# Kernel tuning notes

Measured on AMD Instinct MI355X. Metric: run time of the kernel, lower is better.

## Reference

```python
import jax, jax.numpy as jnp
import numpy as np

B, N, K, NS = 2, 1024, 64, 32          # batch, points, keypoints (top-k), ball-query neighbors
RADIUS = 1.0                            # ball-query radius (sample_and_group)
R_VOX, S_VOX = 2.0, 0.4                 # voxelize search radius / step
NV = int(round(2 * R_VOX / S_VOX)) + 1  # 11 offsets per axis
C = NV ** 3                             # 1331 candidates per keypoint
F = 32                                  # deep feature channels (num_feat)


def _gather(data, idx):
    # data: (B, N, ...) ; idx: (B, ...) int -> (B, idx_shape..., ...)
    return jax.vmap(lambda d, i: d[i])(data, idx)


def setup_inputs() -> dict:
    key = jax.random.key(0)
    ks = jax.random.split(key, 16)
    f = lambda k, s: jax.random.normal(k, s, dtype=jnp.float32)
    return {
        "src_pts": f(ks[0], (B, 6, N)),
        "tgt_pts": f(ks[1], (B, 6, N)),
        "R_init": f(ks[2], (1, 3, 3)),
        "t_init": f(ks[3], (3, 1)),
        # feature-extraction shared MLP (6 -> 32 -> 32)
        "W1": f(ks[4], (6, F)) * 0.4, "b1": jnp.zeros((F,), jnp.float32),
        "W2": f(ks[5], (F, F)) * 0.2, "b2": jnp.zeros((F,), jnp.float32),
        # weighting (saliency) MLP (32 -> 16 -> 1)
        "Ww1": f(ks[6], (F, 16)) * 0.3, "bw1": jnp.zeros((16,), jnp.float32),
        "Ww2": f(ks[7], (16, 1)) * 0.3, "bw2": jnp.zeros((1,), jnp.float32),
        # deep-feature-embedding shared MLP (3+32 -> 32 -> 32)
        "Wd1": f(ks[8], (3 + F, F)) * 0.3, "bd1": jnp.zeros((F,), jnp.float32),
        "Wd2": f(ks[9], (F, F)) * 0.2, "bd2": jnp.zeros((F,), jnp.float32),
    }


def reference(src_pts, tgt_pts, R_init, t_init,
              W1, b1, W2, b2, Ww1, bw1, Ww2, bw2, Wd1, bd1, Wd2, bd2):
    def fe(pts):                                   # shared feature extraction (FE1)
        x = jnp.transpose(pts, (0, 2, 1))          # (B,N,6)
        h = jax.nn.relu(x @ W1 + b1)
        return x[..., :3], jax.nn.relu(h @ W2 + b2)  # xyz (B,N,3), feat (B,N,F)

    def dfe(x):                                    # shared DFE mini-PointNet MLP
        h = jax.nn.relu(x @ Wd1 + bd1)
        return jax.nn.relu(h @ Wd2 + bd2)

    src_xyz_all, src_feat = fe(src_pts)
    tgt_xyz_all, tgt_feat = fe(tgt_pts)

    # ---- weighting layer: per-point saliency, top-K keypoints ----
    score = (jax.nn.relu(src_feat @ Ww1 + bw1) @ Ww2 + bw2)[..., 0]  # (B,N)
    _, key_idx = jax.lax.top_k(score, K)                              # (B,K)

    src_pts_T = jnp.transpose(src_pts, (0, 2, 1))                     # (B,N,6)
    keypts = _gather(src_pts_T, key_idx)                              # (B,K,6)
    kxyz = keypts[..., :3]                                            # (B,K,3)

    # ---- sample_and_group: ball query among keypoints (npoint == K) ----
    sqd = jnp.sum((kxyz[:, :, None] - kxyz[:, None]) ** 2, -1)        # (B,K,K)
    gidx = jnp.broadcast_to(jnp.arange(K), (B, K, K))
    gidx = jnp.where(sqd > RADIUS ** 2, K, gidx)
    gidx = jnp.sort(gidx, -1)[:, :, :NS]
    gidx = jnp.where(gidx == K, gidx[:, :, :1], gidx)                 # (B,K,NS)

    grouped = _gather(kxyz, gidx)                                     # (B,K,NS,3)
    rel = grouped - kxyz[:, :, None]                                  # local coords
    orig_idx = _gather(key_idx, gidx)                                 # (B,K,NS) into N
    keyfeats = _gather(src_feat, orig_idx)                            # (B,K,NS,F)
    src_cat = jnp.concatenate([rel, keyfeats], -1)                    # (B,K,NS,3+F)

    # ---- voxelize: candidate grid around R_init-transformed keypoints ----
    Rm = jnp.broadcast_to(R_init, (B, 3, 3))
    kxyz_t = jnp.einsum('bij,bkj->bki', Rm, kxyz)                     # (B,K,3)
    off = jnp.linspace(-R_VOX, R_VOX, NV, dtype=jnp.float32)
    gx, gy, gz = jnp.meshgrid(off, off, off, indexing='ij')
    grid = jnp.stack([gx, gy, gz], -1).reshape(-1, 3)                 # (C,3)
    cand = kxyz_t[:, :, None, :] + grid                               # (B,K,C,3)

    # ---- 1-NN of each candidate in the target cloud (feature lookup) ----
    cn = jnp.sum(cand ** 2, -1)                                       # (B,K,C)
    tn = jnp.sum(tgt_xyz_all ** 2, -1)                                # (B,N)
    cross = jnp.einsum('bkcd,bnd->bkcn', cand, tgt_xyz_all)           # (B,K,C,N)
    d = cn[..., None] + tn[:, None, None, :] - 2.0 * cross
    nn = jnp.argmin(jax.lax.stop_gradient(d), -1)                     # (B,K,C)
    nn_xyz = _gather(tgt_xyz_all, nn)                                 # (B,K,C,3)
    nn_feat = _gather(tgt_feat, nn)                                   # (B,K,C,F)
    tgt_cat = jnp.concatenate([cand - nn_xyz, nn_feat], -1)           # (B,K,C,3+F)

    # ---- DFE embeddings + corresponding-point generation (CPG) ----
    src_emb = jnp.max(dfe(src_cat), axis=2)                           # (B,K,F)  max over neighbors
    tgt_emb = dfe(tgt_cat)                                            # (B,K,C,F)
    sim = jnp.einsum('bkd,bkcd->bkc', src_emb, tgt_emb)               # (B,K,C)
    w = jax.nn.softmax(sim, -1)
    tgt_vcp = jnp.einsum('bkc,bkcd->bkd', w, cand)                    # (B,K,3)

    return kxyz, tgt_vcp
```

## Files before the change

kernel.cpp:

```cpp
#include <hip/hip_runtime.h>
#include <math.h>

#define BB 2
#define NPTS 1024
#define KK 64
#define NSZ 32
#define CC 1331
#define FF 32
#define RAD2 1.0f
#define NCOL 121
#define NRNG 4

__global__ __launch_bounds__(64)
void k_features(const float* __restrict__ src_pts, const float* __restrict__ tgt_pts,
                const float* __restrict__ W1, const float* __restrict__ b1,
                const float* __restrict__ W2, const float* __restrict__ b2,
                const float* __restrict__ Ww1, const float* __restrict__ bw1,
                const float* __restrict__ Ww2, const float* __restrict__ bw2,
                const float* __restrict__ Wd1, const float* __restrict__ bd1,
                float* __restrict__ src_feat, float* __restrict__ tgt_A,
                float* __restrict__ tgt_m2, float* __restrict__ score)
{
    int gid = blockIdx.x * blockDim.x + threadIdx.x;
    int isTgt = gid >= BB * NPTS;
    int pn = gid & (BB * NPTS - 1);
    int b = pn >> 10, n = pn & 1023;
    const float* pts = isTgt ? tgt_pts : src_pts;
    float p[6];
#pragma unroll
    for (int i = 0; i < 6; i++) p[i] = pts[(b * 6 + i) * NPTS + n];
    float h[FF];
#pragma unroll
    for (int j = 0; j < FF; j++) {
        float a = b1[j];
#pragma unroll
        for (int i = 0; i < 6; i++) a = fmaf(p[i], W1[i * FF + j], a);
        h[j] = fmaxf(a, 0.0f);
    }
    float ft[FF];
#pragma unroll
    for (int j = 0; j < FF; j++) {
        float a = b2[j];
#pragma unroll
        for (int i = 0; i < FF; i++) a = fmaf(h[i], W2[i * FF + j], a);
        ft[j] = fmaxf(a, 0.0f);
    }
    if (isTgt) {
        float x = p[0], y = p[1], z = p[2];
        float4 v; v.x = x; v.y = y; v.z = z; v.w = x * x + y * y + z * z;
        ((float4*)tgt_m2)[b * NPTS + n] = v;
        float av[FF];
#pragma unroll
        for (int j = 0; j < FF; j++) av[j] = bd1[j];
#pragma unroll
        for (int i = 0; i < FF; i++) {
            float fi = ft[i];
#pragma unroll
            for (int j = 0; j < FF; j++)
                av[j] = fmaf(fi, Wd1[(3 + i) * FF + j], av[j]);
        }
#pragma unroll
        for (int j = 0; j < FF; j++) tgt_A[(b * NPTS + n) * FF + j] = av[j];
    } else {
#pragma unroll
        for (int j = 0; j < FF; j++) src_feat[(b * NPTS + n) * FF + j] = ft[j];
        float acc = bw2[0];
#pragma unroll
        for (int j = 0; j < 16; j++) {
            float a = bw1[j];
#pragma unroll
            for (int i = 0; i < FF; i++) a = fmaf(ft[i], Ww1[i * 16 + j], a);
            acc = fmaf(fmaxf(a, 0.0f), Ww2[j], acc);
        }
        score[b * NPTS + n] = acc;
    }
}

__global__ __launch_bounds__(256)
void k_rank(const float* __restrict__ score, const float* __restrict__ src_pts,
            const float* __restrict__ R,
            int* __restrict__ key_idx, float* __restrict__ kxyz,
            float* __restrict__ kxyz_t, float* __restrict__ out_kxyz)
{
    int blk = blockIdx.x;
    int b = blk >> 4;
    int pbase = (blk & 15) << 6;
    int t = threadIdx.x;
    int sub = t & 3;
    int lp = t >> 2;
    int n = pbase + lp;
    __shared__ float sc[NPTS];
    for (int i = t; i < NPTS; i += 256) sc[i] = score[b * NPTS + i];
    __syncthreads();
    float s = sc[n];
    int rank = 0;
#pragma unroll 8
    for (int jj = 0; jj < 256; jj++) {
        int j = (jj << 2) | sub;
        float sj = sc[j];
        bool before = (sj > s) || (sj == s && j < n);
        rank += before ? 1 : 0;
    }
    rank += __shfl_xor(rank, 1, 64);
    rank += __shfl_xor(rank, 2, 64);
    if (sub == 0 && rank < KK) {
        key_idx[b * KK + rank] = n;
        float x = src_pts[(b * 6 + 0) * NPTS + n];
        float y = src_pts[(b * 6 + 1) * NPTS + n];
        float z = src_pts[(b * 6 + 2) * NPTS + n];
        int o = (b * KK + rank) * 3;
        kxyz[o] = x; kxyz[o + 1] = y; kxyz[o + 2] = z;
        out_kxyz[o] = x; out_kxyz[o + 1] = y; out_kxyz[o + 2] = z;
#pragma unroll
        for (int i = 0; i < 3; i++)
            kxyz_t[o + i] = R[i * 3 + 0] * x + R[i * 3 + 1] * y + R[i * 3 + 2] * z;
    }
}

__global__ __launch_bounds__(256)
void k_scan(const float* __restrict__ kxyz_t, const float* __restrict__ tgt_m2,
            const float* __restrict__ kxyz, const int* __restrict__ key_idx,
            const float* __restrict__ src_feat,
            const float* __restrict__ Wd1, const float* __restrict__ bd1,
            const float* __restrict__ Wd2, const float* __restrict__ bd2,
            float2* __restrict__ part, float* __restrict__ src_emb)
{
    int bid = blockIdx.x;
    int bk = bid >> 2, r = bid & 3;
    int b = bk >> 6, kk = bk & 63;
    int t = threadIdx.x;
    int u = t >> 7, lt = t & 127;
    __shared__ float4 P[256];
    __shared__ float2 pbuf[2][NCOL][11];
    __shared__ float kxs[KK][3];
    __shared__ int gidx[NSZ];
    __shared__ float hb[NSZ][FF + 1];
    __shared__ float eb[NSZ][FF + 1];
    P[t] = ((const float4*)tgt_m2)[(b << 10) + (r << 8) + t];
    float kx = kxyz_t[bk * 3 + 0], ky = kxyz_t[bk * 3 + 1], kz = kxyz_t[bk * 3 + 2];
    float kx2 = -2.0f * kx, ky2 = -2.0f * ky, kz2 = -2.0f * kz;
    bool active = lt < NCOL;
    int pc = active ? lt : 0;
    int ixv = pc / 11, iyv = pc - ixv * 11;
    float gx2 = -2.0f * (-2.0f + ixv * 0.4f);
    float gy2 = -2.0f * (-2.0f + iyv * 0.4f);
    float gz2[11];
#pragma unroll
    for (int iz = 0; iz < 11; iz++) gz2[iz] = -2.0f * (-2.0f + iz * 0.4f);
    float best[11]; int bn[11];
#pragma unroll
    for (int iz = 0; iz < 11; iz++) { best[iz] = 3.0e38f; bn[iz] = 0; }
    __syncthreads();
    if (active) {
        const int pb = u << 7;
#pragma unroll 8
        for (int i = 0; i < 128; i++) {
            float4 v = P[pb + i];
            float a = fmaf(kx2, v.x, fmaf(ky2, v.y, fmaf(kz2, v.z, v.w)));
            float e = fmaf(gx2, v.x, fmaf(gy2, v.y, a));
#pragma unroll
            for (int iz = 0; iz < 11; iz++) {
                float d = fmaf(gz2[iz], v.z, e);
                bool l = d < best[iz];
                best[iz] = l ? d : best[iz];
                bn[iz] = l ? i : bn[iz];
            }
        }
#pragma unroll
        for (int iz = 0; iz < 11; iz++)
            pbuf[u][lt][iz] = make_float2(best[iz], __int_as_float(bn[iz] + (u << 7)));
    }
    __syncthreads();
    if (u == 0 && active) {
        int cbase = ((bk << 2) + r) * CC + lt * 11;
#pragma unroll
        for (int iz = 0; iz < 11; iz++) {
            float2 r0 = pbuf[0][lt][iz], r1 = pbuf[1][lt][iz];
            float2 m = (r1.x < r0.x) ? r1 : r0;
            part[cbase + iz] = make_float2(m.x,
                __int_as_float(__float_as_int(m.y) + (r << 8)));
        }
    }
    if (r != 0) return;
    if (t < KK) {
        kxs[t][0] = kxyz[(b * KK + t) * 3 + 0];
        kxs[t][1] = kxyz[(b * KK + t) * 3 + 1];
        kxs[t][2] = kxyz[(b * KK + t) * 3 + 2];
    }
    __syncthreads();
    if (t < KK) {
        float cx = kxs[kk][0], cy = kxs[kk][1], cz = kxs[kk][2];
        float dx = kxs[t][0] - cx, dy = kxs[t][1] - cy, dz = kxs[t][2] - cz;
        float sq = dx * dx + dy * dy + dz * dz;
        unsigned long long mask = __ballot(sq <= RAD2);
        if (t < NSZ) {
            int cnt = __popcll(mask);
            int want = (t < cnt) ? t : 0;
            unsigned long long mm = mask;
            for (int q = 0; q < want; q++) mm &= (mm - 1);
            gidx[t] = __ffsll(mm) - 1;
        }
    }
    __syncthreads();
    {
        int s = t >> 3, jb = (t & 7) << 2;
        int g = gidx[s];
        float cx = kxs[kk][0], cy = kxs[kk][1], cz = kxs[kk][2];
        float xr = kxs[g][0] - cx, yr = kxs[g][1] - cy, zr = kxs[g][2] - cz;
        int orig = key_idx[b * KK + g];
        const float* fz = &src_feat[(b * NPTS + orig) * FF];
        float fr[FF];
#pragma unroll
        for (int i = 0; i < FF; i++) fr[i] = fz[i];
#pragma unroll
        for (int jj = 0; jj < 4; jj++) {
            int j = jb + jj;
            float a = bd1[j];
            a = fmaf(xr, Wd1[0 * FF + j], a);
            a = fmaf(yr, Wd1[1 * FF + j], a);
            a = fmaf(zr, Wd1[2 * FF + j], a);
#pragma unroll
            for (int i = 0; i < FF; i++) a = fmaf(fr[i], Wd1[(3 + i) * FF + j], a);
            hb[s][j] = fmaxf(a, 0.0f);
        }
    }
    __syncthreads();
    {
        int s = t >> 3, jb = (t & 7) << 2;
#pragma unroll
        for (int jj = 0; jj < 4; jj++) {
            int j = jb + jj;
            float a = bd2[j];
#pragma unroll
            for (int i = 0; i < FF; i++) a = fmaf(hb[s][i], Wd2[i * FF + j], a);
            eb[s][j] = fmaxf(a, 0.0f);
        }
    }
    __syncthreads();
    if (t < FF) {
        float m = eb[0][t];
#pragma unroll
        for (int s2 = 1; s2 < NSZ; s2++) m = fmaxf(m, eb[s2][t]);
        src_emb[bk * FF + t] = m;
    }
}

__global__ __launch_bounds__(256)
void k_mlp(const float2* __restrict__ part, const float* __restrict__ kxyz_t,
           const float* __restrict__ tgt_m2, const float* __restrict__ tgt_A,
           const float* __restrict__ src_emb,
           const float* __restrict__ Wd1,
           const float* __restrict__ Wd2, const float* __restrict__ bd2,
           float* __restrict__ sim)
{
    const int NCH = 6;
    int bid = blockIdx.x;
    int chunk = bid % NCH;
    int bk = bid / NCH;
    int b = bk >> 6;
    int t = threadIdx.x;
    int c = chunk * 256 + t;
    int cc = min(c, CC - 1);
    float2 rb = part[(bk << 2) * CC + cc];
#pragma unroll
    for (int r = 1; r < NRNG; r++) {
        float2 o = part[((bk << 2) + r) * CC + cc];
        if (o.x < rb.x) rb = o;
    }
    int nb = __float_as_int(rb.y);
    float4 nv = ((const float4*)tgt_m2)[(b << 10) + nb];
    const float4* az = (const float4*)&tgt_A[((b << 10) + nb) * FF];
    float h[FF];
#pragma unroll
    for (int i = 0; i < FF / 4; i++) {
        float4 v = az[i];
        h[i * 4 + 0] = v.x; h[i * 4 + 1] = v.y; h[i * 4 + 2] = v.z; h[i * 4 + 3] = v.w;
    }
    int ixv = cc / 121, rem = cc - ixv * 121, iyv = rem / 11, izv = rem - iyv * 11;
    float cx = kxyz_t[bk * 3 + 0] + (-2.0f + ixv * 0.4f);
    float cy = kxyz_t[bk * 3 + 1] + (-2.0f + iyv * 0.4f);
    float cz = kxyz_t[bk * 3 + 2] + (-2.0f + izv * 0.4f);
    float x0 = cx - nv.x, x1 = cy - nv.y, x2 = cz - nv.z;
#pragma unroll
    for (int j = 0; j < FF; j++) {
        float a = h[j];
        a = fmaf(x0, Wd1[0 * FF + j], a);
        a = fmaf(x1, Wd1[1 * FF + j], a);
        a = fmaf(x2, Wd1[2 * FF + j], a);
        h[j] = fmaxf(a, 0.0f);
    }
    float sv = 0.0f;
#pragma unroll
    for (int j = 0; j < FF; j++) {
        float a = bd2[j];
#pragma unroll
        for (int i = 0; i < FF; i++) a = fmaf(h[i], Wd2[i * FF + j], a);
        sv = fmaf(fmaxf(a, 0.0f), src_emb[bk * FF + j], sv);
    }
    if (c < CC) sim[bk * CC + c] = sv;
}

__global__ __launch_bounds__(256)
void k_softmax(const float* __restrict__ sim, const float* __restrict__ kxyz_t,
               float* __restrict__ out_vcp)
{
    int bk = blockIdx.x;
    int t = threadIdx.x;
    __shared__ float red[256];
    __shared__ float4 red4[256];
    float kx = kxyz_t[bk * 3 + 0], ky = kxyz_t[bk * 3 + 1], kz = kxyz_t[bk * 3 + 2];
    float lm = -3.0e38f;
    for (int c = t; c < CC; c += 256) lm = fmaxf(lm, sim[bk * CC + c]);
    red[t] = lm;
    __syncthreads();
    for (int s2 = 128; s2 > 0; s2 >>= 1) {
        if (t < s2) red[t] = fmaxf(red[t], red[t + s2]);
        __syncthreads();
    }
    float m = red[0];
    float se = 0.f, sx = 0.f, sy = 0.f, sz = 0.f;
    for (int c = t; c < CC; c += 256) {
        float e = expf(sim[bk * CC + c] - m);
        int ix = c / 121, rem = c - ix * 121, iy = rem / 11, iz = rem - iy * 11;
        float cxx = kx + (-2.0f + ix * 0.4f);
        float cyy = ky + (-2.0f + iy * 0.4f);
        float czz = kz + (-2.0f + iz * 0.4f);
        se += e;
        sx = fmaf(e, cxx, sx);
        sy = fmaf(e, cyy, sy);
        sz = fmaf(e, czz, sz);
    }
    red4[t] = make_float4(se, sx, sy, sz);
    __syncthreads();
    for (int s2 = 128; s2 > 0; s2 >>= 1) {
        if (t < s2) {
            float4 a = red4[t], bq = red4[t + s2];
            red4[t] = make_float4(a.x + bq.x, a.y + bq.y, a.z + bq.z, a.w + bq.w);
        }
        __syncthreads();
    }
    if (t == 0) {
        float4 r = red4[0];
        out_vcp[bk * 3 + 0] = r.y / r.x;
        out_vcp[bk * 3 + 1] = r.z / r.x;
        out_vcp[bk * 3 + 2] = r.w / r.x;
    }
}

extern "C" void kernel_launch(void* const* d_in, const int* in_sizes, int n_in,
                              void* d_out, int out_size, void* d_ws, size_t ws_size,
                              hipStream_t stream)
{
    (void)in_sizes; (void)n_in; (void)out_size; (void)ws_size;
    const float* src_pts = (const float*)d_in[0];
    const float* tgt_pts = (const float*)d_in[1];
    const float* R_init  = (const float*)d_in[2];
    const float* W1  = (const float*)d_in[4];
    const float* b1  = (const float*)d_in[5];
    const float* W2  = (const float*)d_in[6];
    const float* b2  = (const float*)d_in[7];
    const float* Ww1 = (const float*)d_in[8];
    const float* bw1 = (const float*)d_in[9];
    const float* Ww2 = (const float*)d_in[10];
    const float* bw2 = (const float*)d_in[11];
    const float* Wd1 = (const float*)d_in[12];
    const float* bd1 = (const float*)d_in[13];
    const float* Wd2 = (const float*)d_in[14];
    const float* bd2 = (const float*)d_in[15];

    float* ws = (float*)d_ws;
    float* src_feat = ws;
    float* tgt_A    = src_feat + BB * NPTS * FF;
    float* tgt_m2   = tgt_A + BB * NPTS * FF;
    float* score    = tgt_m2 + BB * NPTS * 4;
    int*   key_idx  = (int*)(score + BB * NPTS);
    float* kxyz     = (float*)(key_idx + BB * KK);
    float* kxyz_t   = kxyz + BB * KK * 3;
    float* src_emb  = kxyz_t + BB * KK * 3;
    float* sim      = src_emb + BB * KK * FF;
    float2* part    = (float2*)(sim + BB * KK * CC);

    float* out_kxyz = (float*)d_out;
    float* out_vcp  = out_kxyz + BB * KK * 3;

    k_features<<<64, 64, 0, stream>>>(
        src_pts, tgt_pts, W1, b1, W2, b2, Ww1, bw1, Ww2, bw2, Wd1, bd1,
        src_feat, tgt_A, tgt_m2, score);
    k_rank<<<BB * 16, 256, 0, stream>>>(score, src_pts, R_init,
                                        key_idx, kxyz, kxyz_t, out_kxyz);
    k_scan<<<BB * KK * NRNG, 256, 0, stream>>>(kxyz_t, tgt_m2, kxyz, key_idx,
                                               src_feat, Wd1, bd1, Wd2, bd2,
                                               part, src_emb);
    k_mlp<<<BB * KK * 6, 256, 0, stream>>>(part, kxyz_t, tgt_m2, tgt_A, src_emb,
                                           Wd1, Wd2, bd2, sim);
    k_softmax<<<BB * KK, 256, 0, stream>>>(sim, kxyz_t, out_vcp);
}
```

Before: 66.27 us.

## Fuse softmax partial reductions into MLP kernel with per-chunk online combine

Instead of writing the full similarity array and running a separate softmax kernel, each MLP block computes its own chunk max, exp-sums and weighted coordinate sums in shared memory and writes a small per-chunk record. A tiny final kernel merges the chunk partials with log-sum-exp rescaling to produce the virtual corresponding points. This removes the sim array round trip and the per-keypoint serial softmax block, at the cost of two block reductions inside the MLP kernel.

After: 63.52 us (median of 2 runs). -4.1%, faster.

```diff
diff --git a/kernel.cpp b/kernel.cpp
--- a/kernel.cpp
+++ b/kernel.cpp
@@ -10,6 +10,7 @@
 #define RAD2 1.0f
 #define NCOL 121
 #define NRNG 4
+#define NCH 6
 
 __global__ __launch_bounds__(64)
 void k_features(const float* __restrict__ src_pts, const float* __restrict__ tgt_pts,
@@ -251,9 +252,8 @@
            const float* __restrict__ src_emb,
            const float* __restrict__ Wd1,
            const float* __restrict__ Wd2, const float* __restrict__ bd2,
-           float* __restrict__ sim)
-{
-    const int NCH = 6;
+           float* __restrict__ chunkred)
+{
     int bid = blockIdx.x;
     int chunk = bid % NCH;
     int bk = bid / NCH;
@@ -297,54 +297,54 @@
         for (int i = 0; i < FF; i++) a = fmaf(h[i], Wd2[i * FF + j], a);
         sv = fmaf(fmaxf(a, 0.0f), src_emb[bk * FF + j], sv);
     }
-    if (c < CC) sim[bk * CC + c] = sv;
-}
-
-__global__ __launch_bounds__(256)
-void k_softmax(const float* __restrict__ sim, const float* __restrict__ kxyz_t,
-               float* __restrict__ out_vcp)
-{
-    int bk = blockIdx.x;
-    int t = threadIdx.x;
+    bool valid = (c < CC);
     __shared__ float red[256];
     __shared__ float4 red4[256];
-    float kx = kxyz_t[bk * 3 + 0], ky = kxyz_t[bk * 3 + 1], kz = kxyz_t[bk * 3 + 2];
-    float lm = -3.0e38f;
-    for (int c = t; c < CC; c += 256) lm = fmaxf(lm, sim[bk * CC + c]);
-    red[t] = lm;
+    red[t] = valid ? sv : -3.0e38f;
     __syncthreads();
     for (int s2 = 128; s2 > 0; s2 >>= 1) {
         if (t < s2) red[t] = fmaxf(red[t], red[t + s2]);
         __syncthreads();
     }
-    float m = red[0];
-    float se = 0.f, sx = 0.f, sy = 0.f, sz = 0.f;
-    for (int c = t; c < CC; c += 256) {
-        float e = expf(sim[bk * CC + c] - m);
-        int ix = c / 121, rem = c - ix * 121, iy = rem / 11, iz = rem - iy * 11;
-        float cxx = kx + (-2.0f + ix * 0.4f);
-        float cyy = ky + (-2.0f + iy * 0.4f);
-        float czz = kz + (-2.0f + iz * 0.4f);
-        se += e;
-        sx = fmaf(e, cxx, sx);
-        sy = fmaf(e, cyy, sy);
-        sz = fmaf(e, czz, sz);
-    }
-    red4[t] = make_float4(se, sx, sy, sz);
+    float mc = red[0];
+    float e = valid ? expf(sv - mc) : 0.0f;
+    red4[t] = make_float4(e, e * cx, e * cy, e * cz);
     __syncthreads();
     for (int s2 = 128; s2 > 0; s2 >>= 1) {
         if (t < s2) {
-            float4 a = red4[t], bq = red4[t + s2];
-            red4[t] = make_float4(a.x + bq.x, a.y + bq.y, a.z + bq.z, a.w + bq.w);
+            float4 a2 = red4[t], bq = red4[t + s2];
+            red4[t] = make_float4(a2.x + bq.x, a2.y + bq.y, a2.z + bq.z, a2.w + bq.w);
         }
         __syncthreads();
     }
     if (t == 0) {
-        float4 r = red4[0];
-        out_vcp[bk * 3 + 0] = r.y / r.x;
-        out_vcp[bk * 3 + 1] = r.z / r.x;
-        out_vcp[bk * 3 + 2] = r.w / r.x;
-    }
+        float4 rr = red4[0];
+        float* o = &chunkred[(bk * NCH + chunk) * 8];
+        o[0] = mc; o[1] = rr.x; o[2] = rr.y; o[3] = rr.z; o[4] = rr.w;
+    }
+}
+
+__global__ __launch_bounds__(64)
+void k_final(const float* __restrict__ chunkred, float* __restrict__ out_vcp)
+{
+    int bk = blockIdx.x * 64 + threadIdx.x;
+    if (bk >= BB * KK) return;
+    const float* cr = &chunkred[bk * NCH * 8];
+    float m = cr[0];
+#pragma unroll
+    for (int q = 1; q < NCH; q++) m = fmaxf(m, cr[q * 8]);
+    float S = 0.f, X = 0.f, Y = 0.f, Z = 0.f;
+#pragma unroll
+    for (int q = 0; q < NCH; q++) {
+        float w = expf(cr[q * 8] - m);
+        S = fmaf(cr[q * 8 + 1], w, S);
+        X = fmaf(cr[q * 8 + 2], w, X);
+        Y = fmaf(cr[q * 8 + 3], w, Y);
+        Z = fmaf(cr[q * 8 + 4], w, Z);
+    }
+    out_vcp[bk * 3 + 0] = X / S;
+    out_vcp[bk * 3 + 1] = Y / S;
+    out_vcp[bk * 3 + 2] = Z / S;
 }
 
 extern "C" void kernel_launch(void* const* d_in, const int* in_sizes, int n_in,
@@ -377,8 +377,8 @@
     float* kxyz     = (float*)(key_idx + BB * KK);
     float* kxyz_t   = kxyz + BB * KK * 3;
     float* src_emb  = kxyz_t + BB * KK * 3;
-    float* sim      = src_emb + BB * KK * FF;
-    float2* part    = (float2*)(sim + BB * KK * CC);
+    float* chunkred = src_emb + BB * KK * FF;
+    float2* part    = (float2*)(chunkred + BB * KK * NCH * 8);
 
     float* out_kxyz = (float*)d_out;
     float* out_vcp  = out_kxyz + BB * KK * 3;
@@ -391,7 +391,7 @@
     k_scan<<<BB * KK * NRNG, 256, 0, stream>>>(kxyz_t, tgt_m2, kxyz, key_idx,
                                                src_feat, Wd1, bd1, Wd2, bd2,
                                                part, src_emb);
-    k_mlp<<<BB * KK * 6, 256, 0, stream>>>(part, kxyz_t, tgt_m2, tgt_A, src_emb,
-                                           Wd1, Wd2, bd2, sim);
-    k_softmax<<<BB * KK, 256, 0, stream>>>(sim, kxyz_t, out_vcp);
-}
+    k_mlp<<<BB * KK * NCH, 256, 0, stream>>>(part, kxyz_t, tgt_m2, tgt_A, src_emb,
+                                             Wd1, Wd2, bd2, chunkred);
+    k_final<<<2, 64, 0, stream>>>(chunkred, out_vcp);
+}
```

## Fuse DFE MLP and softmax-weighted sum into one per-keypoint kernel

Applied to the files above, without the earlier changes.

Merges the candidate MLP kernel and the softmax/weighted-centroid kernel into a single kernel with one 512-thread block per keypoint. Each thread evaluates up to three candidates, keeps the similarity scores in registers, and reduces them in shared memory. This removes a kernel launch and the global round-trip of the similarity buffer. In exchange, the grid shrinks from 768 blocks to 128 blocks, so less of the GPU is occupied and each thread does three candidates' MLP work serially.

Measured after the change: 249.0 us. 276% more time.

```diff
diff --git a/kernel.cpp b/kernel.cpp
--- a/kernel.cpp
+++ b/kernel.cpp
@@ -245,94 +245,91 @@
     }
 }
 
-__global__ __launch_bounds__(256)
-void k_mlp(const float2* __restrict__ part, const float* __restrict__ kxyz_t,
+__global__ __launch_bounds__(512)
+void k_vcp(const float2* __restrict__ part, const float* __restrict__ kxyz_t,
            const float* __restrict__ tgt_m2, const float* __restrict__ tgt_A,
            const float* __restrict__ src_emb,
            const float* __restrict__ Wd1,
            const float* __restrict__ Wd2, const float* __restrict__ bd2,
-           float* __restrict__ sim)
-{
-    const int NCH = 6;
-    int bid = blockIdx.x;
-    int chunk = bid % NCH;
-    int bk = bid / NCH;
+           float* __restrict__ out_vcp)
+{
+    int bk = blockIdx.x;
     int b = bk >> 6;
     int t = threadIdx.x;
-    int c = chunk * 256 + t;
-    int cc = min(c, CC - 1);
-    float2 rb = part[(bk << 2) * CC + cc];
-#pragma unroll
-    for (int r = 1; r < NRNG; r++) {
-        float2 o = part[((bk << 2) + r) * CC + cc];
-        if (o.x < rb.x) rb = o;
-    }
-    int nb = __float_as_int(rb.y);
-    float4 nv = ((const float4*)tgt_m2)[(b << 10) + nb];
-    const float4* az = (const float4*)&tgt_A[((b << 10) + nb) * FF];
-    float h[FF];
-#pragma unroll
-    for (int i = 0; i < FF / 4; i++) {
-        float4 v = az[i];
-        h[i * 4 + 0] = v.x; h[i * 4 + 1] = v.y; h[i * 4 + 2] = v.z; h[i * 4 + 3] = v.w;
-    }
-    int ixv = cc / 121, rem = cc - ixv * 121, iyv = rem / 11, izv = rem - iyv * 11;
-    float cx = kxyz_t[bk * 3 + 0] + (-2.0f + ixv * 0.4f);
-    float cy = kxyz_t[bk * 3 + 1] + (-2.0f + iyv * 0.4f);
-    float cz = kxyz_t[bk * 3 + 2] + (-2.0f + izv * 0.4f);
-    float x0 = cx - nv.x, x1 = cy - nv.y, x2 = cz - nv.z;
-#pragma unroll
-    for (int j = 0; j < FF; j++) {
-        float a = h[j];
-        a = fmaf(x0, Wd1[0 * FF + j], a);
-        a = fmaf(x1, Wd1[1 * FF + j], a);
-        a = fmaf(x2, Wd1[2 * FF + j], a);
-        h[j] = fmaxf(a, 0.0f);
-    }
-    float sv = 0.0f;
-#pragma unroll
-    for (int j = 0; j < FF; j++) {
-        float a = bd2[j];
-#pragma unroll
-        for (int i = 0; i < FF; i++) a = fmaf(h[i], Wd2[i * FF + j], a);
-        sv = fmaf(fmaxf(a, 0.0f), src_emb[bk * FF + j], sv);
-    }
-    if (c < CC) sim[bk * CC + c] = sv;
-}
-
-__global__ __launch_bounds__(256)
-void k_softmax(const float* __restrict__ sim, const float* __restrict__ kxyz_t,
-               float* __restrict__ out_vcp)
-{
-    int bk = blockIdx.x;
-    int t = threadIdx.x;
-    __shared__ float red[256];
-    __shared__ float4 red4[256];
+    __shared__ float red[512];
+    __shared__ float4 red4[512];
     float kx = kxyz_t[bk * 3 + 0], ky = kxyz_t[bk * 3 + 1], kz = kxyz_t[bk * 3 + 2];
+    float svp[3], cxp[3], cyp[3], czp[3];
+    bool valp[3];
+#pragma unroll
+    for (int p = 0; p < 3; p++) {
+        int c = p * 512 + t;
+        bool valid = (c < CC);
+        valp[p] = valid;
+        int cc = min(c, CC - 1);
+        float2 rb = part[(bk << 2) * CC + cc];
+#pragma unroll
+        for (int r = 1; r < NRNG; r++) {
+            float2 o = part[((bk << 2) + r) * CC + cc];
+            if (o.x < rb.x) rb = o;
+        }
+        int nb = __float_as_int(rb.y);
+        float4 nv = ((const float4*)tgt_m2)[(b << 10) + nb];
+        const float4* az = (const float4*)&tgt_A[((b << 10) + nb) * FF];
+        float h[FF];
+#pragma unroll
+        for (int i = 0; i < FF / 4; i++) {
+            float4 v = az[i];
+            h[i * 4 + 0] = v.x; h[i * 4 + 1] = v.y;
+            h[i * 4 + 2] = v.z; h[i * 4 + 3] = v.w;
+        }
+        int ixv = cc / 121, rem = cc - ixv * 121, iyv = rem / 11, izv = rem - iyv * 11;
+        float cx = kx + (-2.0f + ixv * 0.4f);
+        float cy = ky + (-2.0f + iyv * 0.4f);
+        float cz = kz + (-2.0f + izv * 0.4f);
+        float x0 = cx - nv.x, x1 = cy - nv.y, x2 = cz - nv.z;
+#pragma unroll
+        for (int j = 0; j < FF; j++) {
+            float a = h[j];
+            a = fmaf(x0, Wd1[0 * FF + j], a);
+            a = fmaf(x1, Wd1[1 * FF + j], a);
+            a = fmaf(x2, Wd1[2 * FF + j], a);
+            h[j] = fmaxf(a, 0.0f);
+        }
+        float sv = 0.0f;
+#pragma unroll
+        for (int j = 0; j < FF; j++) {
+            float a = bd2[j];
+#pragma unroll
+            for (int i = 0; i < FF; i++) a = fmaf(h[i], Wd2[i * FF + j], a);
+            sv = fmaf(fmaxf(a, 0.0f), src_emb[bk * FF + j], sv);
+        }
+        svp[p] = sv; cxp[p] = cx; cyp[p] = cy; czp[p] = cz;
+    }
     float lm = -3.0e38f;
-    for (int c = t; c < CC; c += 256) lm = fmaxf(lm, sim[bk * CC + c]);
+#pragma unroll
+    for (int p = 0; p < 3; p++) if (valp[p]) lm = fmaxf(lm, svp[p]);
     red[t] = lm;
     __syncthreads();
-    for (int s2 = 128; s2 > 0; s2 >>= 1) {
+    for (int s2 = 256; s2 > 0; s2 >>= 1) {
         if (t < s2) red[t] = fmaxf(red[t], red[t + s2]);
         __syncthreads();
     }
     float m = red[0];
-    float se = 0.f, sx = 0.f, sy = 0.f, sz = 0.f;
-    for (int c = t; c < CC; c += 256) {
-        float e = expf(sim[bk * CC + c] - m);
-        int ix = c / 121, rem = c - ix * 121, iy = rem / 11, iz = rem - iy * 11;
-        float cxx = kx + (-2.0f + ix * 0.4f);
-        float cyy = ky + (-2.0f + iy * 0.4f);
-        float czz = kz + (-2.0f + iz * 0.4f);
-        se += e;
-        sx = fmaf(e, cxx, sx);
-        sy = fmaf(e, cyy, sy);
-        sz = fmaf(e, czz, sz);
-    }
-    red4[t] = make_float4(se, sx, sy, sz);
-    __syncthreads();
-    for (int s2 = 128; s2 > 0; s2 >>= 1) {
+    float S = 0.f, X = 0.f, Y = 0.f, Z = 0.f;
+#pragma unroll
+    for (int p = 0; p < 3; p++) {
+        if (valp[p]) {
+            float e = expf(svp[p] - m);
+            S += e;
+            X = fmaf(e, cxp[p], X);
+            Y = fmaf(e, cyp[p], Y);
+            Z = fmaf(e, czp[p], Z);
+        }
+    }
+    red4[t] = make_float4(S, X, Y, Z);
+    __syncthreads();
+    for (int s2 = 256; s2 > 0; s2 >>= 1) {
         if (t < s2) {
             float4 a = red4[t], bq = red4[t + s2];
             red4[t] = make_float4(a.x + bq.x, a.y + bq.y, a.z + bq.z, a.w + bq.w);
@@ -340,10 +337,10 @@
         __syncthreads();
     }
     if (t == 0) {
-        float4 r = red4[0];
-        out_vcp[bk * 3 + 0] = r.y / r.x;
-        out_vcp[bk * 3 + 1] = r.z / r.x;
-        out_vcp[bk * 3 + 2] = r.w / r.x;
+        float4 rr = red4[0];
+        out_vcp[bk * 3 + 0] = rr.y / rr.x;
+        out_vcp[bk * 3 + 1] = rr.z / rr.x;
+        out_vcp[bk * 3 + 2] = rr.w / rr.x;
     }
 }
 
@@ -377,8 +374,7 @@
     float* kxyz     = (float*)(key_idx + BB * KK);
     float* kxyz_t   = kxyz + BB * KK * 3;
     float* src_emb  = kxyz_t + BB * KK * 3;
-    float* sim      = src_emb + BB * KK * FF;
-    float2* part    = (float2*)(sim + BB * KK * CC);
+    float2* part    = (float2*)(src_emb + BB * KK * FF);
 
     float* out_kxyz = (float*)d_out;
     float* out_vcp  = out_kxyz + BB * KK * 3;
@@ -391,7 +387,6 @@
     k_scan<<<BB * KK * NRNG, 256, 0, stream>>>(kxyz_t, tgt_m2, kxyz, key_idx,
                                                src_feat, Wd1, bd1, Wd2, bd2,
                                                part, src_emb);
-    k_mlp<<<BB * KK * 6, 256, 0, stream>>>(part, kxyz_t, tgt_m2, tgt_A, src_emb,
-                                           Wd1, Wd2, bd2, sim);
-    k_softmax<<<BB * KK, 256, 0, stream>>>(sim, kxyz_t, out_vcp);
-}
+    k_vcp<<<BB * KK, 512, 0, stream>>>(part, kxyz_t, tgt_m2, tgt_A, src_emb,
+                                       Wd1, Wd2, bd2, out_vcp);
+}
```
